# Performance work log

Hardware: AMD Instinct MI355X
Metric: run time of the kernel (lower is better)

Reference implementation:

```python
import jax, jax.numpy as jnp
import numpy as np

B, T, D = 8, 512, 512
MAX_DUR = 15          # durations drawn from [0,16) then clamped to >=1
MAX_LEN = T * MAX_DUR # static padded frame length (torch pads to per-batch max)


def setup_inputs() -> dict:
    key = jax.random.key(0)
    kf, kd = jax.random.split(key)
    features = jax.random.normal(kf, (B, T, D), dtype=jnp.float32)
    durations = jax.random.randint(kd, (B, T), 0, 16, dtype=jnp.int32)
    return {"features": features, "durations": durations}


def reference(features, durations):
    """Duration-based length regulation (variable-length expand + pad).

    For each batch b, phoneme t is repeated durations[b,t] times along the
    frame axis; sequences are zero-padded to MAX_LEN. Implemented as a
    vectorized cumsum + searchsorted gather (no per-element host syncs).
    """
    Bv, Tv, Dv = features.shape
    dur = jnp.maximum(durations, 1)               # clamp(min=1) as in forward()
    cum = jnp.cumsum(dur, axis=1)                 # (B, T) exclusive-right frame boundaries
    pos = jnp.arange(MAX_LEN, dtype=cum.dtype)    # (MAX_LEN,)
    # idx[b, n] = source phoneme for output frame n: count of boundaries <= n
    idx = jax.vmap(lambda c: jnp.searchsorted(c, pos, side="right"))(cum)  # (B, MAX_LEN)
    valid = pos[None, :] < cum[:, -1:]            # (B, MAX_LEN) frames within total length
    idx = jnp.minimum(idx, Tv - 1)                # keep gather in-bounds for padded frames
    out = jnp.take_along_axis(features, idx[..., None], axis=1)  # (B, MAX_LEN, D)
    return jnp.where(valid[..., None], out, jnp.zeros((), features.dtype))
```

## Files before the change

### kernel.cpp

```cpp
#include <hip/hip_runtime.h>

#define BB 8
#define TT 512
#define DD 512
#define MAX_LEN 7680
#define FPB 30
#define BPB (MAX_LEN / FPB)

typedef float f32x4 __attribute__((ext_vector_type(4)));

__global__ __launch_bounds__(256) void build_idx_kernel(
    const int2* __restrict__ dur2,
    int*        __restrict__ idx_ws)
{
    __shared__ int ps[256];
    __shared__ int idx_s[MAX_LEN];

    const int t = threadIdx.x;
    const int b = blockIdx.x;

    int2 dd = dur2[b * (TT / 2) + t];
    int d0 = dd.x < 1 ? 1 : dd.x;
    int d1 = dd.y < 1 ? 1 : dd.y;
    ps[t] = d0 + d1;

    for (int j = t; j < MAX_LEN; j += 256) idx_s[j] = -1;
    __syncthreads();

#pragma unroll
    for (int off = 1; off < 256; off <<= 1) {
        int x = (t >= off) ? ps[t - off] : 0;
        __syncthreads();
        ps[t] += x;
        __syncthreads();
    }
    const int incl = ps[t];
    const int s1   = incl - d1;
    const int s0   = s1 - d0;

    for (int k = s0; k < s1; ++k)   idx_s[k] = 2 * t;
    for (int k = s1; k < incl; ++k) idx_s[k] = 2 * t + 1;
    __syncthreads();

    for (int j = t; j < MAX_LEN; j += 256)
        idx_ws[b * MAX_LEN + j] = idx_s[j];
}

__global__ __launch_bounds__(256) void expand_kernel(
    const float4* __restrict__ feat,
    const int*    __restrict__ idx_ws,
    float4*       __restrict__ out)
{
    __shared__ int idx_s[FPB];

    const int t    = threadIdx.x;
    const int b    = blockIdx.x / BPB;
    const int base = (blockIdx.x % BPB) * FPB;

    if (t < FPB) idx_s[t] = idx_ws[b * MAX_LEN + base + t];
    __syncthreads();

    const int lane = t & 127;
    const int sub  = t >> 7;

#pragma unroll
    for (int j = 0; j < FPB; j += 2) {
        const int n   = base + j + sub;
        const int src = idx_s[j + sub];
        float4 val = make_float4(0.f, 0.f, 0.f, 0.f);
        if (src >= 0)
            val = feat[(size_t)(b * TT + src) * (DD / 4) + lane];
        __builtin_nontemporal_store(
            *(const f32x4*)&val,
            (f32x4*)&out[((size_t)b * MAX_LEN + n) * (DD / 4) + lane]);
    }
}

__global__ __launch_bounds__(256) void regulate_kernel(
    const float4* __restrict__ feat,
    const int2*   __restrict__ dur2,
    float4*       __restrict__ out)
{
    __shared__ int cum[TT];
    __shared__ int ps[256];

    const int t    = threadIdx.x;
    const int b    = blockIdx.x / BPB;
    const int base = (blockIdx.x % BPB) * FPB;

    int2 dd = dur2[b * (TT / 2) + t];
    int d0 = dd.x < 1 ? 1 : dd.x;
    int d1 = dd.y < 1 ? 1 : dd.y;
    ps[t] = d0 + d1;
    __syncthreads();
#pragma unroll
    for (int off = 1; off < 256; off <<= 1) {
        int x = (t >= off) ? ps[t - off] : 0;
        __syncthreads();
        ps[t] += x;
        __syncthreads();
    }
    int incl = ps[t];
    cum[2 * t]     = incl - d1;
    cum[2 * t + 1] = incl;
    __syncthreads();

    const int total = cum[TT - 1];
    const int lane  = t & 127;
    const int sub   = t >> 7;

#pragma unroll
    for (int j = 0; j < FPB; j += 2) {
        const int n = base + j + sub;
        float4 val = make_float4(0.f, 0.f, 0.f, 0.f);
        if (n < total) {
            int lo = 0, hi = TT;
#pragma unroll
            for (int s = 0; s < 10; ++s) {
                int mid = (lo + hi) >> 1;
                if (cum[mid] <= n) lo = mid + 1; else hi = mid;
            }
            val = feat[(size_t)(b * TT + lo) * (DD / 4) + lane];
        }
        out[((size_t)b * MAX_LEN + n) * (DD / 4) + lane] = val;
    }
}

extern "C" void kernel_launch(void* const* d_in, const int* in_sizes, int n_in,
                              void* d_out, int out_size, void* d_ws, size_t ws_size,
                              hipStream_t stream) {
    const float* feat;
    const int*   dur;
    if (in_sizes[0] == BB * TT) {
        dur  = (const int*)d_in[0];
        feat = (const float*)d_in[1];
    } else {
        feat = (const float*)d_in[0];
        dur  = (const int*)d_in[1];
    }
    float* out = (float*)d_out;

    const size_t idx_bytes = (size_t)BB * MAX_LEN * sizeof(int);
    if (d_ws != nullptr && ws_size >= idx_bytes) {
        int* idx_ws = (int*)d_ws;
        build_idx_kernel<<<BB, 256, 0, stream>>>((const int2*)dur, idx_ws);
        expand_kernel<<<BB * BPB, 256, 0, stream>>>(
            (const float4*)feat, idx_ws, (float4*)out);
    } else {
        regulate_kernel<<<BB * BPB, 256, 0, stream>>>(
            (const float4*)feat, (const int2*)dur, (float4*)out);
    }
}
```

Baseline: 154.6 us.

## Fuse index build into expand kernel with per-block windowed scatter

Replaces the two-kernel path (one block per batch building a full index map in workspace, then an expand kernel reading it) with a single kernel. Each block recomputes the duration prefix scan and scatters only the frame indices that fall in its own 30-frame window into shared memory, then runs the same gather/nontemporal store loop. This removes a launch, the serial dependency on a low-parallelism 8-block kernel, and the workspace round trip. In exchange every block redoes the 256-thread scan.

```diff
diff --git a/kernel.cpp b/kernel.cpp
--- a/kernel.cpp
+++ b/kernel.cpp
@@ -9,22 +9,24 @@
 
 typedef float f32x4 __attribute__((ext_vector_type(4)));
 
-__global__ __launch_bounds__(256) void build_idx_kernel(
-    const int2* __restrict__ dur2,
-    int*        __restrict__ idx_ws)
+__global__ __launch_bounds__(256) void regulate_kernel(
+    const float4* __restrict__ feat,
+    const int2*   __restrict__ dur2,
+    float4*       __restrict__ out)
 {
     __shared__ int ps[256];
-    __shared__ int idx_s[MAX_LEN];
+    __shared__ int idx_s[FPB];
 
-    const int t = threadIdx.x;
-    const int b = blockIdx.x;
+    const int t    = threadIdx.x;
+    const int b    = blockIdx.x / BPB;
+    const int base = (blockIdx.x % BPB) * FPB;
 
     int2 dd = dur2[b * (TT / 2) + t];
     int d0 = dd.x < 1 ? 1 : dd.x;
     int d1 = dd.y < 1 ? 1 : dd.y;
     ps[t] = d0 + d1;
 
-    for (int j = t; j < MAX_LEN; j += 256) idx_s[j] = -1;
+    if (t < FPB) idx_s[t] = -1;
     __syncthreads();
 
 #pragma unroll
@@ -38,26 +40,15 @@
     const int s1   = incl - d1;
     const int s0   = s1 - d0;
 
-    for (int k = s0; k < s1; ++k)   idx_s[k] = 2 * t;
-    for (int k = s1; k < incl; ++k) idx_s[k] = 2 * t + 1;
-    __syncthreads();
-
-    for (int j = t; j < MAX_LEN; j += 256)
-        idx_ws[b * MAX_LEN + j] = idx_s[j];
-}
-
-__global__ __launch_bounds__(256) void expand_kernel(
-    const float4* __restrict__ feat,
-    const int*    __restrict__ idx_ws,
-    float4*       __restrict__ out)
-{
-    __shared__ int idx_s[FPB];
-
-    const int t    = threadIdx.x;
-    const int b    = blockIdx.x / BPB;
-    const int base = (blockIdx.x % BPB) * FPB;
-
-    if (t < FPB) idx_s[t] = idx_ws[b * MAX_LEN + base + t];
+    const int lim = base + FPB;
+    {
+        int k0 = s0 > base ? s0 : base;
+        int k1 = s1 < lim  ? s1 : lim;
+        for (int k = k0; k < k1; ++k) idx_s[k - base] = 2 * t;
+        int k2 = s1 > base ? s1 : base;
+        int k3 = incl < lim ? incl : lim;
+        for (int k = k2; k < k3; ++k) idx_s[k - base] = 2 * t + 1;
+    }
     __syncthreads();
 
     const int lane = t & 127;
@@ -76,56 +67,6 @@
     }
 }
 
-__global__ __launch_bounds__(256) void regulate_kernel(
-    const float4* __restrict__ feat,
-    const int2*   __restrict__ dur2,
-    float4*       __restrict__ out)
-{
-    __shared__ int cum[TT];
-    __shared__ int ps[256];
-
-    const int t    = threadIdx.x;
-    const int b    = blockIdx.x / BPB;
-    const int base = (blockIdx.x % BPB) * FPB;
-
-    int2 dd = dur2[b * (TT / 2) + t];
-    int d0 = dd.x < 1 ? 1 : dd.x;
-    int d1 = dd.y < 1 ? 1 : dd.y;
-    ps[t] = d0 + d1;
-    __syncthreads();
-#pragma unroll
-    for (int off = 1; off < 256; off <<= 1) {
-        int x = (t >= off) ? ps[t - off] : 0;
-        __syncthreads();
-        ps[t] += x;
-        __syncthreads();
-    }
-    int incl = ps[t];
-    cum[2 * t]     = incl - d1;
-    cum[2 * t + 1] = incl;
-    __syncthreads();
-
-    const int total = cum[TT - 1];
-    const int lane  = t & 127;
-    const int sub   = t >> 7;
-
-#pragma unroll
-    for (int j = 0; j < FPB; j += 2) {
-        const int n = base + j + sub;
-        float4 val = make_float4(0.f, 0.f, 0.f, 0.f);
-        if (n < total) {
-            int lo = 0, hi = TT;
-#pragma unroll
-            for (int s = 0; s < 10; ++s) {
-                int mid = (lo + hi) >> 1;
-                if (cum[mid] <= n) lo = mid + 1; else hi = mid;
-            }
-            val = feat[(size_t)(b * TT + lo) * (DD / 4) + lane];
-        }
-        out[((size_t)b * MAX_LEN + n) * (DD / 4) + lane] = val;
-    }
-}
-
 extern "C" void kernel_launch(void* const* d_in, const int* in_sizes, int n_in,
                               void* d_out, int out_size, void* d_ws, size_t ws_size,
                               hipStream_t stream) {
@@ -140,14 +81,6 @@
     }
     float* out = (float*)d_out;
 
-    const size_t idx_bytes = (size_t)BB * MAX_LEN * sizeof(int);
-    if (d_ws != nullptr && ws_size >= idx_bytes) {
-        int* idx_ws = (int*)d_ws;
-        build_idx_kernel<<<BB, 256, 0, stream>>>((const int2*)dur, idx_ws);
-        expand_kernel<<<BB * BPB, 256, 0, stream>>>(
-            (const float4*)feat, idx_ws, (float4*)out);
-    } else {
-        regulate_kernel<<<BB * BPB, 256, 0, stream>>>(
-            (const float4*)feat, (const int2*)dur, (float4*)out);
-    }
+    regulate_kernel<<<BB * BPB, 256, 0, stream>>>(
+        (const float4*)feat, (const int2*)dur, (float4*)out);
 }
```

Result: no change. 151.6 us (-1.9%).
